# Optimization experiments

Measured on AMD Instinct MI355X. Metric: run time of the kernel, lower is better.

Reference implementation:

```python
import jax, jax.numpy as jnp
import numpy as np


def _cdist_l2(a, b):
    # a: [b,k,D], b: [b,k,D] -> [b,k,k], matches torch.cdist(p=2)
    a2 = jnp.sum(a * a, axis=-1)[:, :, None]
    b2 = jnp.sum(b * b, axis=-1)[:, None, :]
    ab = jnp.einsum('bkd,bjd->bkj', a, b)
    return jnp.sqrt(jnp.maximum(a2 + b2 - 2.0 * ab, 0.0))


def _solve_lsa(cost):
    """Exact Hungarian (Jonker-Volgenant shortest augmenting path, O(n^3))
    on a square cost matrix [n,n]. Returns col_of_row: assigned column per row,
    identical to scipy.optimize.linear_sum_assignment's second return (first is arange).
    1-indexed arrays with a dummy slot 0, classic e-maxx formulation."""
    n = cost.shape[0]
    INF = jnp.float32(1e30)

    def row_body(i, carry):
        u, v, p = carry  # u,v: potentials [n+1]; p[j] = row matched to col j
        way = jnp.zeros(n + 1, jnp.int32)
        minv = jnp.full(n + 1, INF, jnp.float32)
        used = jnp.zeros(n + 1, bool)
        p = p.at[0].set(jnp.int32(i))

        def cond(c):
            j0, p, u, v, way, minv, used = c
            return p[j0] != 0

        def body(c):
            j0, p, u, v, way, minv, used = c
            used = used.at[j0].set(True)
            i0 = p[j0]
            cur = cost[i0 - 1, :] - u[i0] - v[1:]          # reduced costs, cols 1..n
            free = ~used[1:]
            better = free & (cur < minv[1:])
            minv = minv.at[1:].set(jnp.where(better, cur, minv[1:]))
            way = way.at[1:].set(jnp.where(better, j0, way[1:]))
            cand = jnp.where(free, minv[1:], INF)
            jmin = jnp.argmin(cand)
            delta = cand[jmin]
            j1 = (jmin + 1).astype(jnp.int32)
            u = u.at[p].add(jnp.where(used, delta, 0.0))   # u[p[j]] += delta for used j
            v = jnp.where(used, v - delta, v)
            minv = jnp.where(used, minv, minv - delta)
            return (j1, p, u, v, way, minv, used)

        j0 = jnp.int32(0)
        j0, p, u, v, way, minv, used = jax.lax.while_loop(
            cond, body, (j0, p, u, v, way, minv, used))

        # augment along alternating path
        def aug_cond(c):
            j0, p = c
            return j0 != 0

        def aug(c):
            j0, p = c
            j1 = way[j0]
            return (j1, p.at[j0].set(p[j1]))

        _, p = jax.lax.while_loop(aug_cond, aug, (j0, p))
        return (u, v, p)

    u0 = jnp.zeros(n + 1, jnp.float32)
    v0 = jnp.zeros(n + 1, jnp.float32)
    p0 = jnp.zeros(n + 1, jnp.int32)
    _, _, p = jax.lax.fori_loop(1, n + 1, row_body, (u0, v0, p0))
    # p[j] = row of col j  ->  invert to col of row
    col_of_row = jnp.zeros(n, jnp.int32).at[p[1:] - 1].set(jnp.arange(n, dtype=jnp.int32))
    return col_of_row


def setup_inputs() -> dict:
    key = jax.random.key(0)
    k1, k2 = jax.random.split(key)
    B, K, D = 16, 64, 50176  # b, k group masks, h*w = 224*224
    outputs = jax.random.normal(k1, (B, K, D), dtype=jnp.float32)
    targets = jax.random.normal(k2, (B, K, D), dtype=jnp.float32)
    return {"outputs": outputs, "targets": targets}


def reference(outputs, targets):
    # cost_type == 'L2'
    cost_mask = _cdist_l2(outputs, targets)                 # [b,k,k]
    inds2 = jax.vmap(_solve_lsa)(cost_mask)                 # [b,k] matched target idx per pred
    b, k = inds2.shape
    inds = jnp.broadcast_to(jnp.arange(k, dtype=jnp.int32), (b, k))  # scipy row_ind is arange
    return (inds, inds2)
```

## Files before the change

kernel.cpp:

```cpp
#include <hip/hip_runtime.h>

#define DD 50176
#define NB 16
#define NK 64

constexpr int TKK = 16;

template <int KSPLIT>
__global__ __launch_bounds__(256) void gemm_partial(const float* __restrict__ A,
                                                    const float* __restrict__ B,
                                                    float* __restrict__ ws) {
  constexpr int KPS   = DD / KSPLIT;
  constexpr int NTILE = (KPS + TKK - 1) / TKK;
  constexpr int TAILK = KPS - (NTILE - 1) * TKK;
  const int b = blockIdx.y;
  const int w = threadIdx.x >> 6;
  const int lane = threadIdx.x & 63;
  const int s = blockIdx.x * 4 + w;
  const float* Ab = A + (size_t)b * NK * DD;
  const float* Bb = B + (size_t)b * NK * DD;

  __shared__ __align__(16) float lds[4][2][TKK * 64];
  float* As = lds[w][0];
  float* Bs = lds[w][1];

  const int ti = lane >> 3;
  const int tj = lane & 7;
  const int kq = lane & 3;
  const int rr = lane >> 2;

  float c[8][8];
#pragma unroll
  for (int r = 0; r < 8; ++r)
#pragma unroll
    for (int q = 0; q < 8; ++q) c[r][q] = 0.f;
  float a2p[4] = {0.f, 0.f, 0.f, 0.f};
  float b2p[4] = {0.f, 0.f, 0.f, 0.f};
  float4 avr[4], bvr[4];

  const int kbase = s * KPS;
#pragma unroll
  for (int f = 0; f < 4; ++f) {
    const int row = f * 16 + rr;
    avr[f] = *reinterpret_cast<const float4*>(Ab + (size_t)row * DD + kbase + kq * 4);
    bvr[f] = *reinterpret_cast<const float4*>(Bb + (size_t)row * DD + kbase + kq * 4);
  }

  for (int t = 0; t < NTILE; ++t) {
#pragma unroll
    for (int f = 0; f < 4; ++f) {
      const int row = f * 16 + rr;
      const int col = (row + 8 * kq) & 63;
      const float4 av = avr[f], bv = bvr[f];
      As[(kq * 4 + 0) * 64 + col] = av.x;
      As[(kq * 4 + 1) * 64 + col] = av.y;
      As[(kq * 4 + 2) * 64 + col] = av.z;
      As[(kq * 4 + 3) * 64 + col] = av.w;
      Bs[(kq * 4 + 0) * 64 + col] = bv.x;
      Bs[(kq * 4 + 1) * 64 + col] = bv.y;
      Bs[(kq * 4 + 2) * 64 + col] = bv.z;
      Bs[(kq * 4 + 3) * 64 + col] = bv.w;
      a2p[f] = fmaf(av.x, av.x, a2p[f]); a2p[f] = fmaf(av.y, av.y, a2p[f]);
      a2p[f] = fmaf(av.z, av.z, a2p[f]); a2p[f] = fmaf(av.w, av.w, a2p[f]);
      b2p[f] = fmaf(bv.x, bv.x, b2p[f]); b2p[f] = fmaf(bv.y, bv.y, b2p[f]);
      b2p[f] = fmaf(bv.z, bv.z, b2p[f]); b2p[f] = fmaf(bv.w, bv.w, b2p[f]);
    }
    if (t + 1 < NTILE) {
      const int k0 = kbase + (t + 1) * TKK;
      const bool fullnext = (t + 1 < NTILE - 1) || (TAILK == TKK);
      if (fullnext || kq * 4 < TAILK) {
#pragma unroll
        for (int f = 0; f < 4; ++f) {
          const int row = f * 16 + rr;
          avr[f] = *reinterpret_cast<const float4*>(Ab + (size_t)row * DD + k0 + kq * 4);
          bvr[f] = *reinterpret_cast<const float4*>(Bb + (size_t)row * DD + k0 + kq * 4);
        }
      } else {
#pragma unroll
        for (int f = 0; f < 4; ++f) {
          avr[f] = make_float4(0.f, 0.f, 0.f, 0.f);
          bvr[f] = make_float4(0.f, 0.f, 0.f, 0.f);
        }
      }
    }
#pragma unroll 4
    for (int kk = 0; kk < TKK; ++kk) {
      const int g = 8 * (kk >> 2);
      const float4 a0 = *reinterpret_cast<const float4*>(&As[kk * 64 + ((8 * ti + g) & 63)]);
      const float4 a1 = *reinterpret_cast<const float4*>(&As[kk * 64 + ((8 * ti + 4 + g) & 63)]);
      const float4 b0 = *reinterpret_cast<const float4*>(&Bs[kk * 64 + ((8 * tj + g) & 63)]);
      const float4 b1 = *reinterpret_cast<const float4*>(&Bs[kk * 64 + ((8 * tj + 4 + g) & 63)]);
      const float ar[8] = {a0.x, a0.y, a0.z, a0.w, a1.x, a1.y, a1.z, a1.w};
      const float br[8] = {b0.x, b0.y, b0.z, b0.w, b1.x, b1.y, b1.z, b1.w};
#pragma unroll
      for (int r = 0; r < 8; ++r)
#pragma unroll
        for (int q = 0; q < 8; ++q)
          c[r][q] = fmaf(ar[r], br[q], c[r][q]);
    }
  }

  float* Pab = ws + (size_t)(b * KSPLIT + s) * 4096;
#pragma unroll
  for (int r = 0; r < 8; ++r) {
    *reinterpret_cast<float4*>(Pab + (8 * ti + r) * 64 + 8 * tj) =
        make_float4(c[r][0], c[r][1], c[r][2], c[r][3]);
    *reinterpret_cast<float4*>(Pab + (8 * ti + r) * 64 + 8 * tj + 4) =
        make_float4(c[r][4], c[r][5], c[r][6], c[r][7]);
  }

#pragma unroll
  for (int f = 0; f < 4; ++f) {
    a2p[f] += __shfl_xor(a2p[f], 1, 64);
    a2p[f] += __shfl_xor(a2p[f], 2, 64);
    b2p[f] += __shfl_xor(b2p[f], 1, 64);
    b2p[f] += __shfl_xor(b2p[f], 2, 64);
  }
  if (kq == 0) {
    float* Pa2 = ws + (size_t)NB * KSPLIT * 4096 + (size_t)(b * KSPLIT + s) * 64;
    float* Pb2 = Pa2 + (size_t)NB * KSPLIT * 64;
#pragma unroll
    for (int f = 0; f < 4; ++f) {
      Pa2[f * 16 + rr] = a2p[f];
      Pb2[f * 16 + rr] = b2p[f];
    }
  }
}

template <int NSPLIT>
__global__ __launch_bounds__(256) void reduce_cost(const float* __restrict__ ws,
                                                   float* __restrict__ costg) {
  const int slice = blockIdx.x;
  const int b = blockIdx.y;
  const int tid = threadIdx.x;
  __shared__ double a2s[4], b2s[64];
  const size_t pa2 = (size_t)NB * NSPLIT * 4096;
  const size_t pb2 = pa2 + (size_t)NB * NSPLIT * 64;

  if (tid < 64) {
    double s = 0.0;
    for (int sp = 0; sp < NSPLIT; ++sp)
      s += (double)ws[pb2 + (size_t)(b * NSPLIT + sp) * 64 + tid];
    b2s[tid] = s;
  } else if (tid < 68) {
    const int r = slice * 4 + (tid - 64);
    double s = 0.0;
    for (int sp = 0; sp < NSPLIT; ++sp)
      s += (double)ws[pa2 + (size_t)(b * NSPLIT + sp) * 64 + r];
    a2s[tid - 64] = s;
  }

  const int elem = slice * 256 + tid;
  double acc = 0.0;
  for (int sp = 0; sp < NSPLIT; ++sp)
    acc += (double)ws[(size_t)(b * NSPLIT + sp) * 4096 + elem];
  __syncthreads();

  const int ii = tid >> 6;
  const int j = tid & 63;
  const double c2 = a2s[ii] + b2s[j] - 2.0 * acc;
  costg[(size_t)b * 4096 + elem] = (float)sqrt(c2 > 0.0 ? c2 : 0.0);
}

__device__ __forceinline__ float readlane_f(float x, int lane) {
  return __int_as_float(__builtin_amdgcn_readlane(__float_as_int(x), lane));
}

template <int CTRL, int RMASK>
__device__ __forceinline__ float dpp_minf_step(float k) {
  const float o = __int_as_float(__builtin_amdgcn_update_dpp(
      0x7F800000 ,
      __float_as_int(k), CTRL, RMASK, 0xf, false));
  return fminf(o, k);
}
__device__ __forceinline__ float dpp_minf(float k) {
  k = dpp_minf_step<0x111, 0xf>(k);
  k = dpp_minf_step<0x112, 0xf>(k);
  k = dpp_minf_step<0x114, 0xf>(k);
  k = dpp_minf_step<0x118, 0xf>(k);
  k = dpp_minf_step<0x142, 0xa>(k);
  k = dpp_minf_step<0x143, 0xc>(k);
  return readlane_f(k, 63);
}

__global__ __launch_bounds__(64) void lsa_solve(const float* __restrict__ costg,
                                                int* __restrict__ out) {
  const int b = blockIdx.x;
  __shared__ float costd[64 * 64];
  const int tid = threadIdx.x;

  for (int e = tid; e < 4096; e += 64)
    costd[e] = costg[(size_t)b * 4096 + e];
  __syncthreads();

  const int l = tid;
  const float INFF = 1e30f;

  float cmin = costd[l];
  int cargmin = 0;
#pragma unroll 8
  for (int r = 1; r < 64; ++r) {
    const float cv = costd[r * 64 + l];
    if (cv < cmin) { cmin = cv; cargmin = r; }
  }
  float v_l = cmin;
  float u_l = 0.0f;
  int p_l = 0;
  int colof_l = 0;
  unsigned long long rowused = 0ULL;
  for (int j = 0; j < 64; ++j) {
    const int rj = __builtin_amdgcn_readlane(cargmin, j);
    if (!((rowused >> rj) & 1ULL)) {
      rowused |= 1ULL << rj;
      if (l == j) p_l = rj + 1;
      if (l == rj) colof_l = j + 1;
    }
  }
  unsigned long long freemask = ~rowused;

  {
    unsigned long long rm = rowused;
    while (rm) {
      const int ri = __ffsll(rm) - 1;
      rm &= rm - 1;
      const int j1 = __builtin_amdgcn_readlane(colof_l, ri) - 1;
      const float red = (l == j1) ? INFF : (costd[ri * 64 + l] - v_l);
      const float rmin = dpp_minf(red);
      if (l == ri) u_l = rmin;
      if (l == j1) v_l -= rmin;
    }
  }

  for (int pass = 0; pass < 2; ++pass) {
    unsigned long long m = freemask;
    while (m) {
      int ir = __ffsll(m);
      m &= m - 1;
      for (int chain = 0; chain < 8; ++chain) {
        if (!((freemask >> (ir - 1)) & 1ULL)) break;
        const float uir = readlane_f(u_l, ir - 1);
        const float curx = costd[(ir - 1) * 64 + l] - uir - v_l;
        const float u1 = dpp_minf(curx);
        const int j1 = __ffsll(__ballot(curx == u1)) - 1;
        const float cur2 = (l == j1) ? INFF : curx;
        const float u2 = dpp_minf(cur2);
        if (l == ir - 1) u_l = uir + u2;
        const bool strict = (u1 < u2);
        if (strict && l == j1) v_l -= (u2 - u1);
        const int k = __builtin_amdgcn_readlane(p_l, j1);
        if (strict || k == 0) {
          if (l == j1) p_l = ir;
          if (l == ir - 1) colof_l = j1 + 1;
          freemask &= ~(1ULL << (ir - 1));
          if (k != 0) {
            if (l == k - 1) colof_l = 0;
            freemask |= 1ULL << (k - 1);
            if (strict) { ir = k; continue; }
          }
          break;
        } else {
          break;
        }
      }
    }
  }

  for (int i_row = 1; i_row <= 64; ++i_row) {
    if (!((freemask >> (i_row - 1)) & 1ULL)) continue;
    float minv = INFF;
    int way_l = 0;
    bool used = false;
    int j0 = 0;
    const bool irow_hit = (l + 1 == i_row);

    while (true) {
      const int i0 = (j0 == 0) ? i_row : __builtin_amdgcn_readlane(p_l, j0 - 1);
      if (i0 == 0) break;
      if (j0 > 0 && l == j0 - 1) used = true;
      const unsigned long long um = __ballot(used);
      const bool addu = irow_hit ||
                        (colof_l != 0 && ((um >> (colof_l - 1)) & 1ULL));
      const float ui0 = readlane_f(u_l, i0 - 1);
      const float cur = costd[(i0 - 1) * 64 + l] - ui0 - v_l;
      if (!used && cur < minv) { minv = cur; way_l = j0; }
      const float cand = used ? INFF : minv;

      const float delta = dpp_minf(cand);
      const int jmin = __ffsll(__ballot(cand == delta)) - 1;

      if (used) v_l -= delta; else minv -= delta;
      if (addu) u_l += delta;
      j0 = jmin + 1;
    }

    while (j0 != 0) {
      const int j1 = __builtin_amdgcn_readlane(way_l, j0 - 1);
      const int pj1 = (j1 == 0) ? i_row : __builtin_amdgcn_readlane(p_l, j1 - 1);
      if (l == j0 - 1) p_l = pj1;
      if (l == pj1 - 1) colof_l = j0;
      j0 = j1;
    }
  }

  out[b * NK + l] = l;
  out[NB * NK + b * NK + l] = colof_l - 1;
}

extern "C" void kernel_launch(void* const* d_in, const int* in_sizes, int n_in,
                              void* d_out, int out_size, void* d_ws, size_t ws_size,
                              hipStream_t stream) {
  const float* A = (const float*)d_in[0];
  const float* B = (const float*)d_in[1];
  float* ws = (float*)d_ws;
  int* out = (int*)d_out;

  const size_t f128 = (size_t)NB * 128 * 4224;
  const size_t need128 = (f128 + (size_t)NB * 4096) * 4;

  if (ws_size >= need128) {
    float* costg = ws + f128;
    gemm_partial<128><<<dim3(32, NB), 256, 0, stream>>>(A, B, ws);
    reduce_cost<128><<<dim3(16, NB), 256, 0, stream>>>(ws, costg);
    lsa_solve<<<NB, 64, 0, stream>>>(costg, out);
  } else {
    const size_t f64 = (size_t)NB * 64 * 4224;
    float* costg = ws + f64;
    gemm_partial<64><<<dim3(16, NB), 256, 0, stream>>>(A, B, ws);
    reduce_cost<64><<<dim3(16, NB), 256, 0, stream>>>(ws, costg);
    lsa_solve<<<NB, 64, 0, stream>>>(costg, out);
  }
}
```

Baseline: 291.8 us.

## Double K-split to 256 and reduce wave partials in LDS before global write

The GEMM is split across 256 K-slices instead of 128, which doubles the grid to 1024 blocks and raises occupancy with launch bounds of 4. The four waves of each block now sum their 64x64 partials and their norm partials in shared memory, so each block writes one partial set instead of four. This keeps global workspace traffic and reduce_cost work at 64 sets per batch while adding parallelism. The costs are extra barriers and LDS traffic, and the workspace-size fallback path is removed.

```diff
diff --git a/kernel.cpp b/kernel.cpp
--- a/kernel.cpp
+++ b/kernel.cpp
@@ -4,23 +4,27 @@
 #define NB 16
 #define NK 64
 
-constexpr int TKK = 16;
-
-template <int KSPLIT>
-__global__ __launch_bounds__(256) void gemm_partial(const float* __restrict__ A,
-                                                    const float* __restrict__ B,
-                                                    float* __restrict__ ws) {
-  constexpr int KPS   = DD / KSPLIT;
-  constexpr int NTILE = (KPS + TKK - 1) / TKK;
-  constexpr int TAILK = KPS - (NTILE - 1) * TKK;
+constexpr int TKK    = 16;
+constexpr int KSPLIT = 256;
+constexpr int SETS   = KSPLIT / 4;
+constexpr int KPS    = DD / KSPLIT;
+constexpr int NTILE  = (KPS + TKK - 1) / TKK;
+constexpr int TAILK  = KPS - (NTILE - 1) * TKK;
+
+__global__ __launch_bounds__(256, 4) void gemm_partial(const float* __restrict__ A,
+                                                       const float* __restrict__ B,
+                                                       float* __restrict__ ws) {
   const int b = blockIdx.y;
+  const int bx = blockIdx.x;
   const int w = threadIdx.x >> 6;
   const int lane = threadIdx.x & 63;
-  const int s = blockIdx.x * 4 + w;
+  const int s = bx * 4 + w;
   const float* Ab = A + (size_t)b * NK * DD;
   const float* Bb = B + (size_t)b * NK * DD;
 
   __shared__ __align__(16) float lds[4][2][TKK * 64];
+  __shared__ float nb[4][2][64];
+
   float* As = lds[w][0];
   float* Bs = lds[w][1];
 
@@ -100,15 +104,6 @@
     }
   }
 
-  float* Pab = ws + (size_t)(b * KSPLIT + s) * 4096;
-#pragma unroll
-  for (int r = 0; r < 8; ++r) {
-    *reinterpret_cast<float4*>(Pab + (8 * ti + r) * 64 + 8 * tj) =
-        make_float4(c[r][0], c[r][1], c[r][2], c[r][3]);
-    *reinterpret_cast<float4*>(Pab + (8 * ti + r) * 64 + 8 * tj + 4) =
-        make_float4(c[r][4], c[r][5], c[r][6], c[r][7]);
-  }
-
 #pragma unroll
   for (int f = 0; f < 4; ++f) {
     a2p[f] += __shfl_xor(a2p[f], 1, 64);
@@ -117,13 +112,62 @@
     b2p[f] += __shfl_xor(b2p[f], 2, 64);
   }
   if (kq == 0) {
-    float* Pa2 = ws + (size_t)NB * KSPLIT * 4096 + (size_t)(b * KSPLIT + s) * 64;
-    float* Pb2 = Pa2 + (size_t)NB * KSPLIT * 64;
 #pragma unroll
     for (int f = 0; f < 4; ++f) {
-      Pa2[f * 16 + rr] = a2p[f];
-      Pb2[f * 16 + rr] = b2p[f];
-    }
+      nb[w][0][f * 16 + rr] = a2p[f];
+      nb[w][1][f * 16 + rr] = b2p[f];
+    }
+  }
+
+  float* red = &lds[0][0][0];
+  __syncthreads();
+  if (w >= 2) {
+    float* dst = red + (w - 2) * 4096;
+#pragma unroll
+    for (int r = 0; r < 8; ++r) {
+      *reinterpret_cast<float4*>(dst + (8 * ti + r) * 64 + 8 * tj) =
+          make_float4(c[r][0], c[r][1], c[r][2], c[r][3]);
+      *reinterpret_cast<float4*>(dst + (8 * ti + r) * 64 + 8 * tj + 4) =
+          make_float4(c[r][4], c[r][5], c[r][6], c[r][7]);
+    }
+  }
+  __syncthreads();
+  if (w < 2) {
+    const float* src = red + w * 4096;
+#pragma unroll
+    for (int r = 0; r < 8; ++r) {
+      const float4 s0 = *reinterpret_cast<const float4*>(src + (8 * ti + r) * 64 + 8 * tj);
+      const float4 s1 = *reinterpret_cast<const float4*>(src + (8 * ti + r) * 64 + 8 * tj + 4);
+      c[r][0] += s0.x; c[r][1] += s0.y; c[r][2] += s0.z; c[r][3] += s0.w;
+      c[r][4] += s1.x; c[r][5] += s1.y; c[r][6] += s1.z; c[r][7] += s1.w;
+    }
+  }
+  __syncthreads();
+  if (w == 1) {
+#pragma unroll
+    for (int r = 0; r < 8; ++r) {
+      *reinterpret_cast<float4*>(red + (8 * ti + r) * 64 + 8 * tj) =
+          make_float4(c[r][0], c[r][1], c[r][2], c[r][3]);
+      *reinterpret_cast<float4*>(red + (8 * ti + r) * 64 + 8 * tj + 4) =
+          make_float4(c[r][4], c[r][5], c[r][6], c[r][7]);
+    }
+  }
+  __syncthreads();
+  if (w == 0) {
+    float* Pab = ws + (size_t)(b * SETS + bx) * 4096;
+#pragma unroll
+    for (int r = 0; r < 8; ++r) {
+      const float4 s0 = *reinterpret_cast<const float4*>(red + (8 * ti + r) * 64 + 8 * tj);
+      const float4 s1 = *reinterpret_cast<const float4*>(red + (8 * ti + r) * 64 + 8 * tj + 4);
+      *reinterpret_cast<float4*>(Pab + (8 * ti + r) * 64 + 8 * tj) =
+          make_float4(c[r][0] + s0.x, c[r][1] + s0.y, c[r][2] + s0.z, c[r][3] + s0.w);
+      *reinterpret_cast<float4*>(Pab + (8 * ti + r) * 64 + 8 * tj + 4) =
+          make_float4(c[r][4] + s1.x, c[r][5] + s1.y, c[r][6] + s1.z, c[r][7] + s1.w);
+    }
+    float* Pa2 = ws + (size_t)NB * SETS * 4096 + (size_t)(b * SETS + bx) * 64;
+    float* Pb2 = Pa2 + (size_t)NB * SETS * 64;
+    Pa2[lane] = ((nb[0][0][lane] + nb[1][0][lane]) + nb[2][0][lane]) + nb[3][0][lane];
+    Pb2[lane] = ((nb[0][1][lane] + nb[1][1][lane]) + nb[2][1][lane]) + nb[3][1][lane];
   }
 }
 
@@ -314,19 +358,10 @@
   float* ws = (float*)d_ws;
   int* out = (int*)d_out;
 
-  const size_t f128 = (size_t)NB * 128 * 4224;
-  const size_t need128 = (f128 + (size_t)NB * 4096) * 4;
-
-  if (ws_size >= need128) {
-    float* costg = ws + f128;
-    gemm_partial<128><<<dim3(32, NB), 256, 0, stream>>>(A, B, ws);
-    reduce_cost<128><<<dim3(16, NB), 256, 0, stream>>>(ws, costg);
-    lsa_solve<<<NB, 64, 0, stream>>>(costg, out);
-  } else {
-    const size_t f64 = (size_t)NB * 64 * 4224;
-    float* costg = ws + f64;
-    gemm_partial<64><<<dim3(16, NB), 256, 0, stream>>>(A, B, ws);
-    reduce_cost<64><<<dim3(16, NB), 256, 0, stream>>>(ws, costg);
-    lsa_solve<<<NB, 64, 0, stream>>>(costg, out);
-  }
-}
+  const size_t fpart = (size_t)NB * SETS * 4224;
+  float* costg = ws + fpart;
+
+  gemm_partial<<<dim3(SETS, NB), 256, 0, stream>>>(A, B, ws);
+  reduce_cost<SETS><<<dim3(16, NB), 256, 0, stream>>>(ws, costg);
+  lsa_solve<<<NB, 64, 0, stream>>>(costg, out);
+}
```

Measured after the change: 558.5 us. +91.4%, slower.
